# Performance work log

Hardware: AMD Instinct MI355X
Metric: run time of the kernel (lower is better)

The kernel has to match this reference:

```python
import jax, jax.numpy as jnp
from jax import lax
import numpy as np

KERNEL_SIZE = 3
PADDING = 1
STRIDE = 1
DILATION = 1
PATCH_SIZE = 9
DILATION_PATCH = 1

B, C, H, W = 8, 128, 96, 96


def setup_inputs() -> dict:
    key = jax.random.key(0)
    k1, k2, k3 = jax.random.split(key, 3)
    query = jax.random.normal(k1, (B, C, H, W), dtype=jnp.float32)
    key_t = jax.random.normal(k2, (B, C, H, W), dtype=jnp.float32)
    value = jax.random.normal(k3, (B, C, H, W), dtype=jnp.float32)
    return {"query": query, "key": key_t, "value": value}


def _spatial_correlation(query, key):
    """Cost-volume correlation (spatial_correlation_sampler semantics).

    out[b, ph, pw, y, x] = sum_{c,i,j} q[b,c, y*s - p + i*d, x*s - p + j*d]
                                      * k[b,c, same + (ph-r)*dp, same + (pw-r)*dp]
    with out-of-bounds treated as zero. Output: [B, patch, patch, oH, oW].
    """
    b, c, h, w = query.shape
    r = PATCH_SIZE // 2
    dp = DILATION_PATCH
    dk = (KERNEL_SIZE - 1) * DILATION + 1  # dilated kernel extent
    hp, wp = h + 2 * PADDING, w + 2 * PADDING
    oh = (hp - dk) // STRIDE + 1
    ow = (wp - dk) // STRIDE + 1

    q = jnp.pad(query, ((0, 0), (0, 0), (PADDING, PADDING), (PADDING, PADDING)))
    k = jnp.pad(key, ((0, 0), (0, 0),
                      (PADDING + r * dp, PADDING + r * dp),
                      (PADDING + r * dp, PADDING + r * dp)))

    # box-filter kernel: sum over kernel window (no normalization)
    box = jnp.ones((1, 1, KERNEL_SIZE, KERNEL_SIZE), dtype=query.dtype)

    outs = []
    for di in range(PATCH_SIZE):      # fixed small displacement grid (81 iters)
        for dj in range(PATCH_SIZE):
            oy, ox = di * dp, dj * dp
            k_sh = k[:, :, oy:oy + hp, ox:ox + wp]          # shifted key
            prod = jnp.sum(q * k_sh, axis=1, keepdims=True)  # [B,1,Hp,Wp]
            corr = lax.conv_general_dilated(
                prod, box,
                window_strides=(STRIDE, STRIDE),
                padding='VALID',
                rhs_dilation=(DILATION, DILATION),
                dimension_numbers=('NCHW', 'OIHW', 'NCHW'))
            outs.append(corr[:, 0])                          # [B,oH,oW]
    out = jnp.stack(outs, axis=1)  # [B, patch*patch, oH, oW]
    return out.reshape(b, PATCH_SIZE, PATCH_SIZE, oh, ow)


def reference(query, key, value):
    # `value` is accepted (as in the torch module signature) but unused.
    return _spatial_correlation(query, key)
```

## Files before the change

### kernel.cpp

```cpp
#include <hip/hip_runtime.h>


#define BATCH 8
#define CHN   128
#define IMG   96
#define IMG2  (IMG * IMG)
#define TILE  16
#define OTILE 14
#define NC    8
#define NCB   (CHN / NC)
#define KT    24
#define QTP   16
#define NTHR  512
#define NBLK  (7 * 7 * BATCH)

struct Tiles {
  float qs[NC][TILE][QTP];
  float ks[NC][KT][KT];
};

__device__ __forceinline__ void async_ld4(const float* g, float* l) {
  __builtin_amdgcn_global_load_lds((const __attribute__((address_space(1))) unsigned int*)g,
                                   (__attribute__((address_space(3))) unsigned int*)l,
                                   4, 0, 0);
}

template <bool FULL>
__device__ __forceinline__ void issue_stage(const float* __restrict__ qcb,
                                            const float* __restrict__ kcb,
                                            Tiles& tb,
                                            const int (&qoff)[4], const int (&koff)[9],
                                            unsigned qm, unsigned km, int tid) {
  float* qf = &tb.qs[0][0][0] + (tid & ~63);
  float* kf = &tb.ks[0][0][0] + (tid & ~63);
#pragma unroll
  for (int i = 0; i < 4; ++i)
    if (FULL || (qm & (1u << i))) async_ld4(qcb + qoff[i], qf + i * NTHR);
#pragma unroll
  for (int i = 0; i < 9; ++i)
    if (FULL || (km & (1u << i))) async_ld4(kcb + koff[i], kf + i * NTHR);
}

__device__ constexpr int di_lo_o(int OB, int d) {
  const int di = OB / 9 + d;
  return OB > di * 9 ? OB : di * 9;
}
__device__ constexpr int di_hi_o(int OB, int ON, int d) {
  const int di = OB / 9 + d;
  return (OB + ON) < (di * 9 + 9) ? (OB + ON) : (di * 9 + 9);
}
__device__ constexpr bool h_needed(int OB, int ON, int d, int h) {
  const int lo = di_lo_o(OB, d), hi = di_hi_o(OB, ON, d);
  if (lo >= hi) return false;
  const int di = OB / 9 + d;
  const int clo = lo - di * 9, chi = (hi - 1 - di * 9) + 3;
  return (4 * h <= chi) && (4 * h + 3 >= clo);
}

template <int OB, int ON, int d>
__device__ inline void do_row(const Tiles& t, int c, int py, int xg4,
                              const float (&qa)[4], float (&acc)[ON * 4]) {
  if constexpr (di_lo_o(OB, d) < di_hi_o(OB, ON, d)) {
    constexpr int DI0 = OB / 9;
    float kd[12];
    if constexpr (h_needed(OB, ON, d, 0)) *(float4*)&kd[0] = *(const float4*)&t.ks[c][py + DI0 + d][xg4 + 0];
    if constexpr (h_needed(OB, ON, d, 1)) *(float4*)&kd[4] = *(const float4*)&t.ks[c][py + DI0 + d][xg4 + 4];
    if constexpr (h_needed(OB, ON, d, 2)) *(float4*)&kd[8] = *(const float4*)&t.ks[c][py + DI0 + d][xg4 + 8];
#pragma unroll
    for (int oi = 0; oi < ON; ++oi) {
      if ((OB + oi) / 9 == DI0 + d) {
        const int dj = (OB + oi) - ((OB + oi) / 9) * 9;
#pragma unroll
        for (int p = 0; p < 4; ++p)
          acc[oi * 4 + p] = __builtin_fmaf(qa[p], kd[dj + p], acc[oi * 4 + p]);
      }
    }
  }
}

template <int OB, int ON, bool FULL>
__device__ void run(const float* __restrict__ qb, const float* __restrict__ kb,
                    float* __restrict__ out, Tiles* __restrict__ t,
                    const int (&qoff)[4], const int (&koff)[9],
                    unsigned qm, unsigned km,
                    int b, int X0, int Y0, int tid, int lane) {
  const int xg  = lane & 3;
  const int py  = lane >> 2;
  const int xg4 = xg * 4;

  float acc[ON * 4];
#pragma unroll
  for (int i = 0; i < ON * 4; ++i) acc[i] = 0.f;

  issue_stage<FULL>(qb, kb, t[0], qoff, koff, qm, km, tid);
  __syncthreads();

  for (int cb = 0; cb < NCB; ++cb) {
    if (cb + 1 < NCB)
      issue_stage<FULL>(qb + (size_t)(cb + 1) * NC * IMG2,
                        kb + (size_t)(cb + 1) * NC * IMG2,
                        t[(cb + 1) & 1], qoff, koff, qm, km, tid);
    const Tiles& tc = t[cb & 1];
#pragma unroll 2
    for (int c = 0; c < NC; ++c) {
      float qa[4];
      *(float4*)qa = *(const float4*)&tc.qs[c][py][xg4];
      do_row<OB, ON, 0>(tc, c, py, xg4, qa, acc);
      do_row<OB, ON, 1>(tc, c, py, xg4, qa, acc);
      do_row<OB, ON, 2>(tc, c, py, xg4, qa, acc);
    }
    __syncthreads();
  }

  const int srcx = (xg < 3) ? (lane + 1) : lane;
  const int gy   = Y0 + py;
  const bool rowok = (py < OTILE) && (gy < IMG);
  float* obase = out + ((size_t)b * 81 * IMG + gy) * IMG + X0;
#pragma unroll
  for (int oi = 0; oi < ON; ++oi) {
    const float a0 = acc[oi * 4 + 0], a1 = acc[oi * 4 + 1];
    const float a2 = acc[oi * 4 + 2], a3 = acc[oi * 4 + 3];
    const float a0n = __shfl(a0, srcx);
    const float a1n = __shfl(a1, srcx);
    float s0 = a0 + a1 + a2;
    float s1 = a1 + a2 + a3;
    float s2 = a2 + a3 + a0n;
    float s3 = a3 + a0n + a1n;
    s0 += __shfl_down(s0, 4) + __shfl_down(s0, 8);
    s1 += __shfl_down(s1, 4) + __shfl_down(s1, 8);
    s2 += __shfl_down(s2, 4) + __shfl_down(s2, 8);
    s3 += __shfl_down(s3, 4) + __shfl_down(s3, 8);
    if (rowok) {
      const int o = OB + oi;
      float* orow = obase + (size_t)o * IMG * IMG;
      if (xg4 + 0 < OTILE && X0 + xg4 + 0 < IMG) orow[xg4 + 0] = s0;
      if (xg4 + 1 < OTILE && X0 + xg4 + 1 < IMG) orow[xg4 + 1] = s1;
      if (xg4 + 2 < OTILE && X0 + xg4 + 2 < IMG) orow[xg4 + 2] = s2;
      if (xg4 + 3 < OTILE && X0 + xg4 + 3 < IMG) orow[xg4 + 3] = s3;
    }
  }
}

template <bool FULL>
__device__ __forceinline__ void kern_body(const float* __restrict__ q,
                                          const float* __restrict__ k,
                                          float* __restrict__ out, Tiles* t,
                                          int b, int X0, int Y0,
                                          int tid, int lane) {
  unsigned qm = 0, km = 0;
  int qoff[4], koff[9];
#pragma unroll
  for (int i = 0; i < 4; ++i) {
    const int s = i * NTHR + tid;
    const int c = s >> 8, rem = s & 255, rr = rem >> 4, col = rem & 15;
    const int gy = Y0 + rr - 1, gx = X0 + col - 1;
    qoff[i] = c * IMG2 + gy * IMG + gx;
    if ((unsigned)gy < IMG && (unsigned)gx < IMG) qm |= 1u << i; else qoff[i] = 0;
  }
#pragma unroll
  for (int i = 0; i < 9; ++i) {
    const int s = i * NTHR + tid;
    const int c = s / 576, rem = s - c * 576;
    const int r = rem / 24, col = rem - r * 24;
    const int gy = Y0 + r - 5, gx = X0 + col - 5;
    koff[i] = c * IMG2 + gy * IMG + gx;
    if ((unsigned)gy < IMG && (unsigned)gx < IMG) km |= 1u << i; else koff[i] = 0;
  }

  if constexpr (!FULL) {
    float* qf0 = &t[0].qs[0][0][0]; float* qf1 = &t[1].qs[0][0][0];
    float* kf0 = &t[0].ks[0][0][0]; float* kf1 = &t[1].ks[0][0][0];
#pragma unroll
    for (int i = 0; i < 4; ++i)
      if (!(qm & (1u << i))) { qf0[i * NTHR + tid] = 0.f; qf1[i * NTHR + tid] = 0.f; }
#pragma unroll
    for (int i = 0; i < 9; ++i)
      if (!(km & (1u << i))) { kf0[i * NTHR + tid] = 0.f; kf1[i * NTHR + tid] = 0.f; }
  }

  const float* qb = q + (size_t)b * CHN * IMG2;
  const float* kb = k + (size_t)b * CHN * IMG2;

  const int w = tid >> 6;
  if (w == 0)      run<0,  11, FULL>(qb, kb, out, t, qoff, koff, qm, km, b, X0, Y0, tid, lane);
  else if (w == 1) run<11, 10, FULL>(qb, kb, out, t, qoff, koff, qm, km, b, X0, Y0, tid, lane);
  else if (w == 2) run<21, 10, FULL>(qb, kb, out, t, qoff, koff, qm, km, b, X0, Y0, tid, lane);
  else if (w == 3) run<31, 10, FULL>(qb, kb, out, t, qoff, koff, qm, km, b, X0, Y0, tid, lane);
  else if (w == 4) run<41, 10, FULL>(qb, kb, out, t, qoff, koff, qm, km, b, X0, Y0, tid, lane);
  else if (w == 5) run<51, 10, FULL>(qb, kb, out, t, qoff, koff, qm, km, b, X0, Y0, tid, lane);
  else if (w == 6) run<61, 10, FULL>(qb, kb, out, t, qoff, koff, qm, km, b, X0, Y0, tid, lane);
  else             run<71, 10, FULL>(qb, kb, out, t, qoff, koff, qm, km, b, X0, Y0, tid, lane);
}

__global__ __launch_bounds__(NTHR, 4) void spatial_corr_kernel(const float* __restrict__ q,
                                                               const float* __restrict__ k,
                                                               float* __restrict__ out) {
  __shared__ Tiles t[2];
  const int tid  = threadIdx.x;
  const int lane = tid & 63;

  int id = blockIdx.x;
  id = (id & 7) * 49 + (id >> 3);
  const int bx = id % 7; id /= 7;
  const int by = id % 7; id /= 7;
  const int b  = id;
  const int X0 = bx * OTILE;
  const int Y0 = by * OTILE;

  const bool full = (bx >= 1) && (bx <= 5) && (by >= 1) && (by <= 5);
  if (full) kern_body<true >(q, k, out, t, b, X0, Y0, tid, lane);
  else      kern_body<false>(q, k, out, t, b, X0, Y0, tid, lane);
}

extern "C" void kernel_launch(void* const* d_in, const int* in_sizes, int n_in,
                              void* d_out, int out_size, void* d_ws, size_t ws_size,
                              hipStream_t stream) {
  const float* q = (const float*)d_in[0];
  const float* k = (const float*)d_in[1];
  float* out = (float*)d_out;
  dim3 grid(NBLK);
  dim3 block(NTHR);
  hipLaunchKernelGGL(spatial_corr_kernel, grid, block, 0, stream, q, k, out);
}
```

Baseline: 232.1 us.

## Use nine waves, one per displacement row, and simplify key tile loading

```diff
diff --git a/kernel.cpp b/kernel.cpp
--- a/kernel.cpp
+++ b/kernel.cpp
@@ -10,12 +10,14 @@
 #define NC    8
 #define NCB   (CHN / NC)
 #define KT    24
-#define QTP   16
-#define NTHR  512
+#define NTHR  576
 #define NBLK  (7 * 7 * BATCH)
 
+#define QFL   (NC * TILE * TILE)
+#define KFL   (NC * KT * KT)
+
 struct Tiles {
-  float qs[NC][TILE][QTP];
+  float qs[NC][TILE][TILE];
   float ks[NC][KT][KT];
 };
 
@@ -25,89 +27,101 @@
                                    4, 0, 0);
 }
 
-template <bool FULL>
 __device__ __forceinline__ void issue_stage(const float* __restrict__ qcb,
                                             const float* __restrict__ kcb,
-                                            Tiles& tb,
-                                            const int (&qoff)[4], const int (&koff)[9],
-                                            unsigned qm, unsigned km, int tid) {
+                                            Tiles& tb, const int (&qoff)[4],
+                                            int koff, unsigned qm, bool kok, int tid) {
   float* qf = &tb.qs[0][0][0] + (tid & ~63);
   float* kf = &tb.ks[0][0][0] + (tid & ~63);
 #pragma unroll
   for (int i = 0; i < 4; ++i)
-    if (FULL || (qm & (1u << i))) async_ld4(qcb + qoff[i], qf + i * NTHR);
+    if (qm & (1u << i)) async_ld4(qcb + qoff[i], qf + i * NTHR);
+  if (kok) {
 #pragma unroll
-  for (int i = 0; i < 9; ++i)
-    if (FULL || (km & (1u << i))) async_ld4(kcb + koff[i], kf + i * NTHR);
-}
-
-__device__ constexpr int di_lo_o(int OB, int d) {
-  const int di = OB / 9 + d;
-  return OB > di * 9 ? OB : di * 9;
-}
-__device__ constexpr int di_hi_o(int OB, int ON, int d) {
-  const int di = OB / 9 + d;
-  return (OB + ON) < (di * 9 + 9) ? (OB + ON) : (di * 9 + 9);
-}
-__device__ constexpr bool h_needed(int OB, int ON, int d, int h) {
-  const int lo = di_lo_o(OB, d), hi = di_hi_o(OB, ON, d);
-  if (lo >= hi) return false;
-  const int di = OB / 9 + d;
-  const int clo = lo - di * 9, chi = (hi - 1 - di * 9) + 3;
-  return (4 * h <= chi) && (4 * h + 3 >= clo);
-}
-
-template <int OB, int ON, int d>
-__device__ inline void do_row(const Tiles& t, int c, int py, int xg4,
-                              const float (&qa)[4], float (&acc)[ON * 4]) {
-  if constexpr (di_lo_o(OB, d) < di_hi_o(OB, ON, d)) {
-    constexpr int DI0 = OB / 9;
-    float kd[12];
-    if constexpr (h_needed(OB, ON, d, 0)) *(float4*)&kd[0] = *(const float4*)&t.ks[c][py + DI0 + d][xg4 + 0];
-    if constexpr (h_needed(OB, ON, d, 1)) *(float4*)&kd[4] = *(const float4*)&t.ks[c][py + DI0 + d][xg4 + 4];
-    if constexpr (h_needed(OB, ON, d, 2)) *(float4*)&kd[8] = *(const float4*)&t.ks[c][py + DI0 + d][xg4 + 8];
-#pragma unroll
-    for (int oi = 0; oi < ON; ++oi) {
-      if ((OB + oi) / 9 == DI0 + d) {
-        const int dj = (OB + oi) - ((OB + oi) / 9) * 9;
-#pragma unroll
-        for (int p = 0; p < 4; ++p)
-          acc[oi * 4 + p] = __builtin_fmaf(qa[p], kd[dj + p], acc[oi * 4 + p]);
-      }
-    }
+    for (int i = 0; i < 8; ++i)
+      async_ld4(kcb + (size_t)i * IMG2 + koff, kf + i * NTHR);
   }
 }
 
-template <int OB, int ON, bool FULL>
-__device__ void run(const float* __restrict__ qb, const float* __restrict__ kb,
-                    float* __restrict__ out, Tiles* __restrict__ t,
-                    const int (&qoff)[4], const int (&koff)[9],
-                    unsigned qm, unsigned km,
-                    int b, int X0, int Y0, int tid, int lane) {
+__global__ __launch_bounds__(NTHR, 5) void spatial_corr_kernel(const float* __restrict__ q,
+                                                               const float* __restrict__ k,
+                                                               float* __restrict__ out) {
+  __shared__ Tiles t[2];
+  const int tid  = threadIdx.x;
+  const int w    = tid >> 6;
+  const int lane = tid & 63;
+
+  int id = blockIdx.x;
+  id = (id & 7) * 49 + (id >> 3);
+  const int bx = id % 7; id /= 7;
+  const int by = id % 7; id /= 7;
+  const int b  = id;
+  const int X0 = bx * OTILE;
+  const int Y0 = by * OTILE;
+
+  unsigned qm = 0;
+  int qoff[4];
+#pragma unroll
+  for (int i = 0; i < 4; ++i) {
+    const int s = i * NTHR + tid;
+    const int c = s >> 8, rem = s & 255, rr = rem >> 4, col = rem & 15;
+    const int gy = Y0 + rr - 1, gx = X0 + col - 1;
+    qoff[i] = c * IMG2 + gy * IMG + gx;
+    const bool ok = (s < QFL) && ((unsigned)gy < IMG) && ((unsigned)gx < IMG);
+    if (ok) qm |= 1u << i; else qoff[i] = 0;
+  }
+  const int kr = tid / KT, kc = tid - kr * KT;
+  const int kgy = Y0 + kr - 5, kgx = X0 + kc - 5;
+  const bool kok = ((unsigned)kgy < IMG) && ((unsigned)kgx < IMG);
+  const int koff = kok ? (kgy * IMG + kgx) : 0;
+
+  {
+    float* qf0 = &t[0].qs[0][0][0]; float* qf1 = &t[1].qs[0][0][0];
+    float* kf0 = &t[0].ks[0][0][0]; float* kf1 = &t[1].ks[0][0][0];
+#pragma unroll
+    for (int i = 0; i < 4; ++i) {
+      const int s = i * NTHR + tid;
+      if (s < QFL && !(qm & (1u << i))) { qf0[s] = 0.f; qf1[s] = 0.f; }
+    }
+    if (!kok) {
+#pragma unroll
+      for (int i = 0; i < 8; ++i) { kf0[i * NTHR + tid] = 0.f; kf1[i * NTHR + tid] = 0.f; }
+    }
+  }
+
+  const float* qb = q + (size_t)b * CHN * IMG2;
+  const float* kb = k + (size_t)b * CHN * IMG2;
+
   const int xg  = lane & 3;
   const int py  = lane >> 2;
   const int xg4 = xg * 4;
 
-  float acc[ON * 4];
+  float acc[36];
 #pragma unroll
-  for (int i = 0; i < ON * 4; ++i) acc[i] = 0.f;
+  for (int i = 0; i < 36; ++i) acc[i] = 0.f;
 
-  issue_stage<FULL>(qb, kb, t[0], qoff, koff, qm, km, tid);
+  issue_stage(qb, kb, t[0], qoff, koff, qm, kok, tid);
   __syncthreads();
 
   for (int cb = 0; cb < NCB; ++cb) {
     if (cb + 1 < NCB)
-      issue_stage<FULL>(qb + (size_t)(cb + 1) * NC * IMG2,
-                        kb + (size_t)(cb + 1) * NC * IMG2,
-                        t[(cb + 1) & 1], qoff, koff, qm, km, tid);
+      issue_stage(qb + (size_t)(cb + 1) * NC * IMG2,
+                  kb + (size_t)(cb + 1) * NC * IMG2,
+                  t[(cb + 1) & 1], qoff, koff, qm, kok, tid);
     const Tiles& tc = t[cb & 1];
 #pragma unroll 2
     for (int c = 0; c < NC; ++c) {
       float qa[4];
       *(float4*)qa = *(const float4*)&tc.qs[c][py][xg4];
-      do_row<OB, ON, 0>(tc, c, py, xg4, qa, acc);
-      do_row<OB, ON, 1>(tc, c, py, xg4, qa, acc);
-      do_row<OB, ON, 2>(tc, c, py, xg4, qa, acc);
+      float kd[12];
+      *(float4*)&kd[0] = *(const float4*)&tc.ks[c][py + w][xg4 + 0];
+      *(float4*)&kd[4] = *(const float4*)&tc.ks[c][py + w][xg4 + 4];
+      *(float4*)&kd[8] = *(const float4*)&tc.ks[c][py + w][xg4 + 8];
+#pragma unroll
+      for (int dj = 0; dj < 9; ++dj)
+#pragma unroll
+        for (int p = 0; p < 4; ++p)
+          acc[dj * 4 + p] = __builtin_fmaf(qa[p], kd[dj + p], acc[dj * 4 + p]);
     }
     __syncthreads();
   }
@@ -117,9 +131,9 @@
   const bool rowok = (py < OTILE) && (gy < IMG);
   float* obase = out + ((size_t)b * 81 * IMG + gy) * IMG + X0;
 #pragma unroll
-  for (int oi = 0; oi < ON; ++oi) {
-    const float a0 = acc[oi * 4 + 0], a1 = acc[oi * 4 + 1];
-    const float a2 = acc[oi * 4 + 2], a3 = acc[oi * 4 + 3];
+  for (int dj = 0; dj < 9; ++dj) {
+    const float a0 = acc[dj * 4 + 0], a1 = acc[dj * 4 + 1];
+    const float a2 = acc[dj * 4 + 2], a3 = acc[dj * 4 + 3];
     const float a0n = __shfl(a0, srcx);
     const float a1n = __shfl(a1, srcx);
     float s0 = a0 + a1 + a2;
@@ -131,85 +145,14 @@
     s2 += __shfl_down(s2, 4) + __shfl_down(s2, 8);
     s3 += __shfl_down(s3, 4) + __shfl_down(s3, 8);
     if (rowok) {
-      const int o = OB + oi;
-      float* orow = obase + (size_t)o * IMG * IMG;
+      const int o = w * 9 + dj;
+      float* orow = obase + (size_t)o * IMG2;
       if (xg4 + 0 < OTILE && X0 + xg4 + 0 < IMG) orow[xg4 + 0] = s0;
       if (xg4 + 1 < OTILE && X0 + xg4 + 1 < IMG) orow[xg4 + 1] = s1;
       if (xg4 + 2 < OTILE && X0 + xg4 + 2 < IMG) orow[xg4 + 2] = s2;
       if (xg4 + 3 < OTILE && X0 + xg4 + 3 < IMG) orow[xg4 + 3] = s3;
     }
   }
-}
-
-template <bool FULL>
-__device__ __forceinline__ void kern_body(const float* __restrict__ q,
-                                          const float* __restrict__ k,
-                                          float* __restrict__ out, Tiles* t,
-                                          int b, int X0, int Y0,
-                                          int tid, int lane) {
-  unsigned qm = 0, km = 0;
-  int qoff[4], koff[9];
-#pragma unroll
-  for (int i = 0; i < 4; ++i) {
-    const int s = i * NTHR + tid;
-    const int c = s >> 8, rem = s & 255, rr = rem >> 4, col = rem & 15;
-    const int gy = Y0 + rr - 1, gx = X0 + col - 1;
-    qoff[i] = c * IMG2 + gy * IMG + gx;
-    if ((unsigned)gy < IMG && (unsigned)gx < IMG) qm |= 1u << i; else qoff[i] = 0;
-  }
-#pragma unroll
-  for (int i = 0; i < 9; ++i) {
-    const int s = i * NTHR + tid;
-    const int c = s / 576, rem = s - c * 576;
-    const int r = rem / 24, col = rem - r * 24;
-    const int gy = Y0 + r - 5, gx = X0 + col - 5;
-    koff[i] = c * IMG2 + gy * IMG + gx;
-    if ((unsigned)gy < IMG && (unsigned)gx < IMG) km |= 1u << i; else koff[i] = 0;
-  }
-
-  if constexpr (!FULL) {
-    float* qf0 = &t[0].qs[0][0][0]; float* qf1 = &t[1].qs[0][0][0];
-    float* kf0 = &t[0].ks[0][0][0]; float* kf1 = &t[1].ks[0][0][0];
-#pragma unroll
-    for (int i = 0; i < 4; ++i)
-      if (!(qm & (1u << i))) { qf0[i * NTHR + tid] = 0.f; qf1[i * NTHR + tid] = 0.f; }
-#pragma unroll
-    for (int i = 0; i < 9; ++i)
-      if (!(km & (1u << i))) { kf0[i * NTHR + tid] = 0.f; kf1[i * NTHR + tid] = 0.f; }
-  }
-
-  const float* qb = q + (size_t)b * CHN * IMG2;
-  const float* kb = k + (size_t)b * CHN * IMG2;
-
-  const int w = tid >> 6;
-  if (w == 0)      run<0,  11, FULL>(qb, kb, out, t, qoff, koff, qm, km, b, X0, Y0, tid, lane);
-  else if (w == 1) run<11, 10, FULL>(qb, kb, out, t, qoff, koff, qm, km, b, X0, Y0, tid, lane);
-  else if (w == 2) run<21, 10, FULL>(qb, kb, out, t, qoff, koff, qm, km, b, X0, Y0, tid, lane);
-  else if (w == 3) run<31, 10, FULL>(qb, kb, out, t, qoff, koff, qm, km, b, X0, Y0, tid, lane);
-  else if (w == 4) run<41, 10, FULL>(qb, kb, out, t, qoff, koff, qm, km, b, X0, Y0, tid, lane);
-  else if (w == 5) run<51, 10, FULL>(qb, kb, out, t, qoff, koff, qm, km, b, X0, Y0, tid, lane);
-  else if (w == 6) run<61, 10, FULL>(qb, kb, out, t, qoff, koff, qm, km, b, X0, Y0, tid, lane);
-  else             run<71, 10, FULL>(qb, kb, out, t, qoff, koff, qm, km, b, X0, Y0, tid, lane);
-}
-
-__global__ __launch_bounds__(NTHR, 4) void spatial_corr_kernel(const float* __restrict__ q,
-                                                               const float* __restrict__ k,
-                                                               float* __restrict__ out) {
-  __shared__ Tiles t[2];
-  const int tid  = threadIdx.x;
-  const int lane = tid & 63;
-
-  int id = blockIdx.x;
-  id = (id & 7) * 49 + (id >> 3);
-  const int bx = id % 7; id /= 7;
-  const int by = id % 7; id /= 7;
-  const int b  = id;
-  const int X0 = bx * OTILE;
-  const int Y0 = by * OTILE;
-
-  const bool full = (bx >= 1) && (bx <= 5) && (by >= 1) && (by <= 5);
-  if (full) kern_body<true >(q, k, out, t, b, X0, Y0, tid, lane);
-  else      kern_body<false>(q, k, out, t, b, X0, Y0, tid, lane);
 }
 
 extern "C" void kernel_launch(void* const* d_in, const int* in_sizes, int n_in,
```

Result: slower. 243.3 us (+4.8%).
